# Kernel tuning notes

Hardware: AMD Instinct MI355X
Metric: run time of the kernel (lower is better)

## Reference

```python
import jax, jax.numpy as jnp
import numpy as np

B, N, C = 16, 1024, 256

def setup_inputs() -> dict:
    key = jax.random.key(0)
    kq, kk, kv, km, kd = jax.random.split(key, 5)
    query = jax.random.normal(kq, (B, N, C), dtype=jnp.float32)
    key_t = jax.random.normal(kk, (B, N, C), dtype=jnp.float32)
    value = jax.random.normal(kv, (B, N, C), dtype=jnp.float32)
    mask = jax.random.randint(km, (B, N, N), 0, 2).astype(jnp.bool_)
    dis = jax.random.normal(kd, (B, N, N), dtype=jnp.float32)
    return {"query": query, "key": key_t, "value": value, "mask": mask, "dis": dis}

def reference(query, key, value, mask, dis):
    # scores = Q K^T + dis, then scale, mask, softmax, @ V
    scores = jnp.einsum('bqc,bkc->bqk', query, key)
    scores = (scores + dis) / jnp.sqrt(jnp.asarray(query.shape[-1], query.dtype))
    scores = jnp.where(mask, -jnp.inf, scores)
    p_attn = jax.nn.softmax(scores, axis=-1)
    p_val = jnp.einsum('bqk,bkc->bqc', p_attn, value)
    return (p_val, p_attn)
```

## Files before the change

kernel.cpp:

```cpp
#include <hip/hip_runtime.h>
#include <stdint.h>

#define B_ 16
#define N_ 1024
#define C_ 256
#define PSTRIDE 1032
#define WBUF 16640

typedef __attribute__((ext_vector_type(8))) short short8;
typedef __attribute__((ext_vector_type(4))) float f32x4;
typedef __attribute__((ext_vector_type(4))) int i32x4;

__device__ __forceinline__ short f2bf(float f) {
  uint32_t u = __builtin_bit_cast(uint32_t, f);
  u += 0x7fffu + ((u >> 16) & 1u);
  return (short)(u >> 16);
}

__device__ __forceinline__ void g2l16(const void* gptr, void* lptr) {
  __builtin_amdgcn_global_load_lds(
      (const __attribute__((address_space(1))) uint32_t*)gptr,
      (__attribute__((address_space(3))) uint32_t*)lptr, 16, 0, 0);
}

#define WC_VM0   0x0F70
#define WC_VM8   0x0F78

__global__ __launch_bounds__(256) void prep_kernel(const float* __restrict__ K,
                                                   const float* __restrict__ V,
                                                   short* __restrict__ Kbf,
                                                   short* __restrict__ Vt) {
  int bx = blockIdx.x;
  if (bx < 2048) {
    size_t i = (size_t)bx * 256 + threadIdx.x;
    const float4* p = (const float4*)(K + i * 8);
    float4 a = p[0], b = p[1];
    short8 r;
    r[0] = f2bf(a.x); r[1] = f2bf(a.y); r[2] = f2bf(a.z); r[3] = f2bf(a.w);
    r[4] = f2bf(b.x); r[5] = f2bf(b.y); r[6] = f2bf(b.z); r[7] = f2bf(b.w);
    *(short8*)(Kbf + i * 8) = r;
  } else {
    bx -= 2048;
    __shared__ short t[64][72];
    int b = bx >> 6;
    int nb = (bx & 15) * 64;
    int cb = ((bx >> 4) & 3) * 64;
    int tx = threadIdx.x & 15;
    int ty = threadIdx.x >> 4;
#pragma unroll
    for (int i = 0; i < 4; i++) {
      int n = ty + 16 * i;
      float4 v = *(const float4*)&V[((size_t)b * N_ + nb + n) * C_ + cb + tx * 4];
      t[tx * 4 + 0][n] = f2bf(v.x);
      t[tx * 4 + 1][n] = f2bf(v.y);
      t[tx * 4 + 2][n] = f2bf(v.z);
      t[tx * 4 + 3][n] = f2bf(v.w);
    }
    __syncthreads();
    int n0 = (threadIdx.x & 7) * 8;
    int c0 = threadIdx.x >> 3;
#pragma unroll
    for (int i = 0; i < 2; i++) {
      int c = c0 + 32 * i;
      short8 s = *(const short8*)&t[c][n0];
      *(short8*)&Vt[((size_t)b * C_ + cb + c) * N_ + nb + n0] = s;
    }
  }
}

__global__ __launch_bounds__(256) void attn_kernel(
    const short* __restrict__ Kbf, const short* __restrict__ Vt,
    const float* __restrict__ Qf32, const float* __restrict__ dis,
    const int* __restrict__ mask, float* __restrict__ p_attn,
    float* __restrict__ p_val) {
  __shared__ char smem[4 * WBUF];
  __shared__ float redm[4][16];
  __shared__ float reds[4][16];

  int gid = blockIdx.x;
  int b = gid & 15;
  int q0 = (gid >> 4) * 16;
  int tid = threadIdx.x;
  int w = tid >> 6;
  int lane = tid & 63;
  int l15 = lane & 15;
  int quad = lane >> 4;

  char* kbuf = smem + w * WBUF;
  short* P_lds = (short*)smem;

  short8 qf[8];
  const float* Qp = Qf32 + ((size_t)b * N_ + q0 + l15) * C_ + quad * 8;
#pragma unroll
  for (int cs = 0; cs < 8; cs++) {
    float4 a = *(const float4*)(Qp + cs * 32);
    float4 c = *(const float4*)(Qp + cs * 32 + 4);
    short8 r;
    r[0] = f2bf(a.x); r[1] = f2bf(a.y); r[2] = f2bf(a.z); r[3] = f2bf(a.w);
    r[4] = f2bf(c.x); r[5] = f2bf(c.y); r[6] = f2bf(c.z); r[7] = f2bf(c.w);
    qf[cs] = r;
  }

  f32x4 z = {0.f, 0.f, 0.f, 0.f};
  f32x4 acc[16];
#pragma unroll
  for (int i = 0; i < 16; i++) acc[i] = z;

  const short* Kp = Kbf + ((size_t)b * N_ + w * 256) * C_;

#define STAGE_K(kt, half)                                                  \
  {                                                                        \
    _Pragma("unroll") for (int p = 0; p < 8; p++)                          \
        g2l16(Kp + ((kt) * 16 + 2 * p) * 256 + lane * 8,                   \
              kbuf + (half) * 8320 + p * 1040);                            \
  }
#define CONSUME_K(kt, half)                                                \
  {                                                                        \
    _Pragma("unroll") for (int cs = 0; cs < 8; cs++) {                     \
      short8 kf = *(const short8*)(kbuf + (half) * 8320 + (l15 >> 1) * 1040 \
                                   + (l15 & 1) * 512 + quad * 16 + cs * 64); \
      acc[kt] = __builtin_amdgcn_mfma_f32_16x16x32_bf16(kf, qf[cs],        \
                                                        acc[kt], 0, 0, 0); \
    }                                                                      \
  }

  STAGE_K(0, 0);
#pragma unroll
  for (int kt = 0; kt < 15; kt++) {
    STAGE_K(kt + 1, (kt + 1) & 1);
    __builtin_amdgcn_s_waitcnt(WC_VM8);
    CONSUME_K(kt, kt & 1);
  }
  __builtin_amdgcn_s_waitcnt(WC_VM0);
  CONSUME_K(15, 1);

  const float* Dp = dis + ((size_t)b * N_ + q0) * N_ + w * 256;
#pragma unroll
  for (int r = 0; r < 16; r++)
    g2l16(Dp + (size_t)r * N_ + lane * 4, kbuf + r * 1040);
  __builtin_amdgcn_s_waitcnt(WC_VM0);
#pragma unroll
  for (int kt = 0; kt < 16; kt++) {
    f32x4 dv = *(const f32x4*)(kbuf + l15 * 1040 + kt * 64 + quad * 16);
#pragma unroll
    for (int r = 0; r < 4; r++) acc[kt][r] = (acc[kt][r] + dv[r]) * 0.0625f;
  }

  const int* Mp = mask + ((size_t)b * N_ + q0) * N_ + w * 256;
#pragma unroll
  for (int r = 0; r < 16; r++)
    g2l16(Mp + (size_t)r * N_ + lane * 4, kbuf + r * 1040);
  __builtin_amdgcn_s_waitcnt(WC_VM0);
  float m = -3.0e38f;
#pragma unroll
  for (int kt = 0; kt < 16; kt++) {
    i32x4 mv = *(const i32x4*)(kbuf + l15 * 1040 + kt * 64 + quad * 16);
#pragma unroll
    for (int r = 0; r < 4; r++) {
      acc[kt][r] = mv[r] ? -3.0e38f : acc[kt][r];
      m = fmaxf(m, acc[kt][r]);
    }
  }

  m = fmaxf(m, __shfl_xor(m, 16));
  m = fmaxf(m, __shfl_xor(m, 32));
  if (lane < 16) redm[w][lane] = m;
  __syncthreads();
  float M = fmaxf(fmaxf(redm[0][l15], redm[1][l15]),
                  fmaxf(redm[2][l15], redm[3][l15]));

  float sum = 0.f;
#pragma unroll
  for (int kt = 0; kt < 16; kt++)
#pragma unroll
    for (int r = 0; r < 4; r++) {
      float e = __expf(acc[kt][r] - M);
      acc[kt][r] = e;
      sum += e;
    }
  sum += __shfl_xor(sum, 16);
  sum += __shfl_xor(sum, 32);
  if (lane < 16) reds[w][lane] = sum;
  __syncthreads();
  float inv = 1.0f / (reds[0][l15] + reds[1][l15] + reds[2][l15] + reds[3][l15]);

  size_t base = ((size_t)b * N_ + q0 + l15) * N_ + w * 256 + quad * 4;
#pragma unroll
  for (int kt = 0; kt < 16; kt++) {
    float4 p;
    p.x = acc[kt][0] * inv;
    p.y = acc[kt][1] * inv;
    p.z = acc[kt][2] * inv;
    p.w = acc[kt][3] * inv;
    *(float4*)(p_attn + base + (size_t)kt * 16) = p;
    short4 pb;
    pb.x = f2bf(p.x); pb.y = f2bf(p.y); pb.z = f2bf(p.z); pb.w = f2bf(p.w);
    *(short4*)&P_lds[l15 * PSTRIDE + w * 256 + kt * 16 + quad * 4] = pb;
  }
  __syncthreads();

  f32x4 o[4];
#pragma unroll
  for (int i = 0; i < 4; i++) o[i] = z;
  const short* Vp = Vt + ((size_t)b * C_ + w * 64 + l15) * N_ + quad * 8;

#pragma unroll 4
  for (int ks = 0; ks < N_; ks += 32) {
    short8 a = *(const short8*)&P_lds[l15 * PSTRIDE + ks + quad * 8];
#pragma unroll
    for (int ct = 0; ct < 4; ct++) {
      short8 bv = *(const short8*)(Vp + (size_t)ct * 16 * N_ + ks);
      o[ct] = __builtin_amdgcn_mfma_f32_16x16x32_bf16(a, bv, o[ct], 0, 0, 0);
    }
  }

#pragma unroll
  for (int ct = 0; ct < 4; ct++)
#pragma unroll
    for (int r = 0; r < 4; r++)
      p_val[((size_t)b * N_ + q0 + quad * 4 + r) * C_ + w * 64 + ct * 16 + l15] =
          o[ct][r];
}

extern "C" void kernel_launch(void* const* d_in, const int* in_sizes, int n_in,
                              void* d_out, int out_size, void* d_ws, size_t ws_size,
                              hipStream_t stream) {
  const float* Q   = (const float*)d_in[0];
  const float* K   = (const float*)d_in[1];
  const float* V   = (const float*)d_in[2];
  const int* mask  = (const int*)d_in[3];
  const float* dis = (const float*)d_in[4];

  float* out = (float*)d_out;
  float* p_val  = out;
  float* p_attn = out + (size_t)B_ * N_ * C_;

  const size_t nelem = (size_t)B_ * N_ * C_;
  short* Kbf = (short*)d_ws;
  short* Vt  = Kbf + nelem;

  prep_kernel<<<dim3(3072), 256, 0, stream>>>(K, V, Kbf, Vt);
  attn_kernel<<<dim3(B_ * (N_ / 16)), 256, 0, stream>>>(Kbf, Vt, Q, dis, mask,
                                                        p_attn, p_val);
}
```

Before: 294.6 us.

## Fuse masked exp into QK loop without max subtraction, defer normalization

Result: slower. 331.8 us (+12.6%).

```diff
diff --git a/kernel.cpp b/kernel.cpp
--- a/kernel.cpp
+++ b/kernel.cpp
@@ -4,27 +4,20 @@
 #define B_ 16
 #define N_ 1024
 #define C_ 256
-#define PSTRIDE 1032
-#define WBUF 16640
+#define EST 1032
 
 typedef __attribute__((ext_vector_type(8))) short short8;
 typedef __attribute__((ext_vector_type(4))) float f32x4;
-typedef __attribute__((ext_vector_type(4))) int i32x4;
 
 __device__ __forceinline__ short f2bf(float f) {
   uint32_t u = __builtin_bit_cast(uint32_t, f);
   u += 0x7fffu + ((u >> 16) & 1u);
   return (short)(u >> 16);
 }
-
-__device__ __forceinline__ void g2l16(const void* gptr, void* lptr) {
-  __builtin_amdgcn_global_load_lds(
-      (const __attribute__((address_space(1))) uint32_t*)gptr,
-      (__attribute__((address_space(3))) uint32_t*)lptr, 16, 0, 0);
-}
-
-#define WC_VM0   0x0F70
-#define WC_VM8   0x0F78
+__device__ __forceinline__ float bf2f(short s) {
+  uint32_t u = ((uint32_t)(uint16_t)s) << 16;
+  return __builtin_bit_cast(float, u);
+}
 
 __global__ __launch_bounds__(256) void prep_kernel(const float* __restrict__ K,
                                                    const float* __restrict__ V,
@@ -73,21 +66,17 @@
     const float* __restrict__ Qf32, const float* __restrict__ dis,
     const int* __restrict__ mask, float* __restrict__ p_attn,
     float* __restrict__ p_val) {
-  __shared__ char smem[4 * WBUF];
-  __shared__ float redm[4][16];
+  __shared__ short E[16 * EST];
   __shared__ float reds[4][16];
 
   int gid = blockIdx.x;
-  int b = gid & 15;
-  int q0 = (gid >> 4) * 16;
+  int b = gid >> 6;
+  int q0 = (gid & 63) * 16;
   int tid = threadIdx.x;
   int w = tid >> 6;
   int lane = tid & 63;
   int l15 = lane & 15;
   int quad = lane >> 4;
-
-  char* kbuf = smem + w * WBUF;
-  short* P_lds = (short*)smem;
 
   short8 qf[8];
   const float* Qp = Qf32 + ((size_t)b * N_ + q0 + l15) * C_ + quad * 8;
@@ -101,104 +90,71 @@
     qf[cs] = r;
   }
 
+  const short* Kp = Kbf + ((size_t)b * N_ + w * 256) * C_;
+  const float* Dp = dis + ((size_t)b * N_ + q0 + l15) * N_ + w * 256 + quad * 4;
+  const int* Mp = mask + ((size_t)b * N_ + q0 + l15) * N_ + w * 256 + quad * 4;
+
+  float Lp = 0.f;
+  float4 dv[2];
+  int4 mv[2];
+  dv[0] = *(const float4*)(Dp);
+  mv[0] = *(const int4*)(Mp);
+  dv[1] = *(const float4*)(Dp + 16);
+  mv[1] = *(const int4*)(Mp + 16);
+
+#pragma unroll
+  for (int kt = 0; kt < 16; kt++) {
+    float4 d_c = dv[kt & 1];
+    int4 m_c = mv[kt & 1];
+    if (kt < 14) {
+      dv[kt & 1] = *(const float4*)(Dp + (kt + 2) * 16);
+      mv[kt & 1] = *(const int4*)(Mp + (kt + 2) * 16);
+    }
+    short8 kf[8];
+#pragma unroll
+    for (int cs = 0; cs < 8; cs++)
+      kf[cs] = *(const short8*)(Kp + ((size_t)(kt * 16 + l15)) * C_ + cs * 32 + quad * 8);
+    f32x4 acc = {0.f, 0.f, 0.f, 0.f};
+#pragma unroll
+    for (int cs = 0; cs < 8; cs++)
+      acc = __builtin_amdgcn_mfma_f32_16x16x32_bf16(kf[cs], qf[cs], acc, 0, 0, 0);
+
+    float e0 = m_c.x ? 0.f : __expf((acc[0] + d_c.x) * 0.0625f);
+    float e1 = m_c.y ? 0.f : __expf((acc[1] + d_c.y) * 0.0625f);
+    float e2 = m_c.z ? 0.f : __expf((acc[2] + d_c.z) * 0.0625f);
+    float e3 = m_c.w ? 0.f : __expf((acc[3] + d_c.w) * 0.0625f);
+    Lp += (e0 + e1) + (e2 + e3);
+    short4 eb;
+    eb.x = f2bf(e0); eb.y = f2bf(e1); eb.z = f2bf(e2); eb.w = f2bf(e3);
+    *(short4*)&E[l15 * EST + w * 256 + kt * 16 + quad * 4] = eb;
+  }
+
+  Lp += __shfl_xor(Lp, 16);
+  Lp += __shfl_xor(Lp, 32);
+  if (lane < 16) reds[w][lane] = Lp;
+  __syncthreads();
+
+  float invq = 1.0f / (reds[0][l15] + reds[1][l15] + reds[2][l15] + reds[3][l15]);
+  float* Pp = p_attn + ((size_t)b * N_ + q0 + l15) * N_ + w * 256 + quad * 4;
+#pragma unroll
+  for (int kt = 0; kt < 16; kt++) {
+    short4 eb = *(const short4*)&E[l15 * EST + w * 256 + kt * 16 + quad * 4];
+    float4 p;
+    p.x = bf2f(eb.x) * invq;
+    p.y = bf2f(eb.y) * invq;
+    p.z = bf2f(eb.z) * invq;
+    p.w = bf2f(eb.w) * invq;
+    *(float4*)(Pp + kt * 16) = p;
+  }
+
+  float invo[4];
+#pragma unroll
+  for (int r = 0; r < 4; r++) {
+    int q = quad * 4 + r;
+    invo[r] = 1.0f / (reds[0][q] + reds[1][q] + reds[2][q] + reds[3][q]);
+  }
+
   f32x4 z = {0.f, 0.f, 0.f, 0.f};
-  f32x4 acc[16];
-#pragma unroll
-  for (int i = 0; i < 16; i++) acc[i] = z;
-
-  const short* Kp = Kbf + ((size_t)b * N_ + w * 256) * C_;
-
-#define STAGE_K(kt, half)                                                  \
-  {                                                                        \
-    _Pragma("unroll") for (int p = 0; p < 8; p++)                          \
-        g2l16(Kp + ((kt) * 16 + 2 * p) * 256 + lane * 8,                   \
-              kbuf + (half) * 8320 + p * 1040);                            \
-  }
-#define CONSUME_K(kt, half)                                                \
-  {                                                                        \
-    _Pragma("unroll") for (int cs = 0; cs < 8; cs++) {                     \
-      short8 kf = *(const short8*)(kbuf + (half) * 8320 + (l15 >> 1) * 1040 \
-                                   + (l15 & 1) * 512 + quad * 16 + cs * 64); \
-      acc[kt] = __builtin_amdgcn_mfma_f32_16x16x32_bf16(kf, qf[cs],        \
-                                                        acc[kt], 0, 0, 0); \
-    }                                                                      \
-  }
-
-  STAGE_K(0, 0);
-#pragma unroll
-  for (int kt = 0; kt < 15; kt++) {
-    STAGE_K(kt + 1, (kt + 1) & 1);
-    __builtin_amdgcn_s_waitcnt(WC_VM8);
-    CONSUME_K(kt, kt & 1);
-  }
-  __builtin_amdgcn_s_waitcnt(WC_VM0);
-  CONSUME_K(15, 1);
-
-  const float* Dp = dis + ((size_t)b * N_ + q0) * N_ + w * 256;
-#pragma unroll
-  for (int r = 0; r < 16; r++)
-    g2l16(Dp + (size_t)r * N_ + lane * 4, kbuf + r * 1040);
-  __builtin_amdgcn_s_waitcnt(WC_VM0);
-#pragma unroll
-  for (int kt = 0; kt < 16; kt++) {
-    f32x4 dv = *(const f32x4*)(kbuf + l15 * 1040 + kt * 64 + quad * 16);
-#pragma unroll
-    for (int r = 0; r < 4; r++) acc[kt][r] = (acc[kt][r] + dv[r]) * 0.0625f;
-  }
-
-  const int* Mp = mask + ((size_t)b * N_ + q0) * N_ + w * 256;
-#pragma unroll
-  for (int r = 0; r < 16; r++)
-    g2l16(Mp + (size_t)r * N_ + lane * 4, kbuf + r * 1040);
-  __builtin_amdgcn_s_waitcnt(WC_VM0);
-  float m = -3.0e38f;
-#pragma unroll
-  for (int kt = 0; kt < 16; kt++) {
-    i32x4 mv = *(const i32x4*)(kbuf + l15 * 1040 + kt * 64 + quad * 16);
-#pragma unroll
-    for (int r = 0; r < 4; r++) {
-      acc[kt][r] = mv[r] ? -3.0e38f : acc[kt][r];
-      m = fmaxf(m, acc[kt][r]);
-    }
-  }
-
-  m = fmaxf(m, __shfl_xor(m, 16));
-  m = fmaxf(m, __shfl_xor(m, 32));
-  if (lane < 16) redm[w][lane] = m;
-  __syncthreads();
-  float M = fmaxf(fmaxf(redm[0][l15], redm[1][l15]),
-                  fmaxf(redm[2][l15], redm[3][l15]));
-
-  float sum = 0.f;
-#pragma unroll
-  for (int kt = 0; kt < 16; kt++)
-#pragma unroll
-    for (int r = 0; r < 4; r++) {
-      float e = __expf(acc[kt][r] - M);
-      acc[kt][r] = e;
-      sum += e;
-    }
-  sum += __shfl_xor(sum, 16);
-  sum += __shfl_xor(sum, 32);
-  if (lane < 16) reds[w][lane] = sum;
-  __syncthreads();
-  float inv = 1.0f / (reds[0][l15] + reds[1][l15] + reds[2][l15] + reds[3][l15]);
-
-  size_t base = ((size_t)b * N_ + q0 + l15) * N_ + w * 256 + quad * 4;
-#pragma unroll
-  for (int kt = 0; kt < 16; kt++) {
-    float4 p;
-    p.x = acc[kt][0] * inv;
-    p.y = acc[kt][1] * inv;
-    p.z = acc[kt][2] * inv;
-    p.w = acc[kt][3] * inv;
-    *(float4*)(p_attn + base + (size_t)kt * 16) = p;
-    short4 pb;
-    pb.x = f2bf(p.x); pb.y = f2bf(p.y); pb.z = f2bf(p.z); pb.w = f2bf(p.w);
-    *(short4*)&P_lds[l15 * PSTRIDE + w * 256 + kt * 16 + quad * 4] = pb;
-  }
-  __syncthreads();
-
   f32x4 o[4];
 #pragma unroll
   for (int i = 0; i < 4; i++) o[i] = z;
@@ -206,7 +162,7 @@
 
 #pragma unroll 4
   for (int ks = 0; ks < N_; ks += 32) {
-    short8 a = *(const short8*)&P_lds[l15 * PSTRIDE + ks + quad * 8];
+    short8 a = *(const short8*)&E[l15 * EST + ks + quad * 8];
 #pragma unroll
     for (int ct = 0; ct < 4; ct++) {
       short8 bv = *(const short8*)(Vp + (size_t)ct * 16 * N_ + ks);
@@ -219,7 +175,7 @@
 #pragma unroll
     for (int r = 0; r < 4; r++)
       p_val[((size_t)b * N_ + q0 + quad * 4 + r) * C_ + w * 64 + ct * 16 + l15] =
-          o[ct][r];
+          o[ct][r] * invo[r];
 }
 
 extern "C" void kernel_launch(void* const* d_in, const int* in_sizes, int n_in,
```
